# Kernel optimization log

Hardware: AMD Instinct MI355X
Metric: run time of the kernel (lower is better)

Reference implementation:

```python
import jax, jax.numpy as jnp
import numpy as np

NUM_ITERATIONS = 3


def _squash(s):
    # Faithful to the torch code: squash over dim=2 of s_j [B,1,nu,us,1],
    # which is the num_units axis. In our [B, nu, us] layout that is axis=1.
    mag_sq = jnp.sum(s ** 2, axis=1, keepdims=True)  # [B,1,us]
    mag = jnp.sqrt(mag_sq)
    return mag_sq / (1.0 + mag_sq) * (s / mag)


def setup_inputs() -> dict:
    key = jax.random.key(0)
    k1, k2 = jax.random.split(key)
    B, in_units, in_channels, num_units, unit_size = 256, 8, 1152, 10, 16
    x = jax.random.normal(k1, (B, in_units, in_channels), dtype=jnp.float32)
    W = jax.random.normal(k2, (1, in_channels, num_units, unit_size, in_units), dtype=jnp.float32)
    return {"x": x, "W": W}


def reference(x, W):
    B = x.shape[0]
    W0 = W[0]  # [ic, nu, us, iu]
    ic, nu = W0.shape[0], W0.shape[1]
    xt = jnp.swapaxes(x, 1, 2)  # [B, ic, iu]
    # u_hat = W @ x per (batch, in_channel, out_unit): [B, ic, nu, us]
    u_hat = jnp.einsum('cdui,bci->bcdu', W0, xt)
    b_ij = jnp.zeros((ic, nu), dtype=x.dtype)
    v = None
    for _ in range(NUM_ITERATIONS):
        c_ij = jax.nn.softmax(b_ij, axis=0)              # softmax over in_channels
        s_j = jnp.einsum('cd,bcdu->bdu', c_ij, u_hat)    # [B, nu, us]
        v = _squash(s_j)                                 # [B, nu, us]
        # agreement: <u_hat, v> over unit_size, mean over batch -> [ic, nu]
        agree = jnp.einsum('bcdu,bdu->cd', u_hat, v) / B
        b_ij = b_ij + agree
    return v  # [B, num_units, unit_size]
```

## Files before the change

### kernel.cpp

```cpp
#include <hip/hip_runtime.h>
#include <math.h>

#define B_  256
#define IU  8
#define IC  1152
#define NU  10
#define US  16
#define CCH 9
#define NCH 128
#define BT  64
#define NBLK 512
#define SPSTRIDE ((size_t)NCH * B_ * NU * US)

__device__ __forceinline__ float gld(const float* p) {
    return __hip_atomic_load(p, __ATOMIC_RELAXED, __HIP_MEMORY_SCOPE_AGENT);
}
__device__ __forceinline__ void gst(float* p, float v) {
    __hip_atomic_store(p, v, __ATOMIC_RELAXED, __HIP_MEMORY_SCOPE_AGENT);
}
__device__ __forceinline__ unsigned uld(const unsigned* p) {
    return __hip_atomic_load(p, __ATOMIC_RELAXED, __HIP_MEMORY_SCOPE_AGENT);
}
__device__ __forceinline__ void ust(unsigned* p, unsigned v) {
    __hip_atomic_store(p, v, __ATOMIC_RELAXED, __HIP_MEMORY_SCOPE_AGENT);
}

__device__ __forceinline__ void gridbar(unsigned* bar) {
    __syncthreads();
    if (threadIdx.x == 0) {
        const int bid = blockIdx.x;
        const int leaf = bid >> 3;
        const int mid  = bid >> 6;
        unsigned* myR1 = bar + (96 + leaf) * 32;
        unsigned g = uld(myR1);
        unsigned a = __hip_atomic_fetch_add(bar + leaf * 32, 1u,
                                            __ATOMIC_RELAXED, __HIP_MEMORY_SCOPE_AGENT);
        if (a == 7u) {
            ust(bar + leaf * 32, 0u);
            unsigned b2 = __hip_atomic_fetch_add(bar + (64 + mid) * 32, 1u,
                                                 __ATOMIC_RELAXED, __HIP_MEMORY_SCOPE_AGENT);
            if (b2 == 7u) {
                ust(bar + (64 + mid) * 32, 0u);
                unsigned c2 = __hip_atomic_fetch_add(bar + 72 * 32, 1u,
                                                     __ATOMIC_RELAXED, __HIP_MEMORY_SCOPE_AGENT);
                if (c2 == 7u) {
                    ust(bar + 72 * 32, 0u);
#pragma unroll
                    for (int k = 0; k < 8; k++)
                        ust(bar + (80 + k) * 32, g + 1u);
                }
                while (uld(bar + (80 + mid) * 32) == g)
                    __builtin_amdgcn_s_sleep(8);
#pragma unroll
                for (int j = 0; j < 8; j++)
                    ust(bar + (96 + mid * 8 + j) * 32, g + 1u);
            }
        }
        while (uld(myR1) == g)
            __builtin_amdgcn_s_sleep(16);
    }
    __syncthreads();
}

__global__ __launch_bounds__(256, 2) void mega(const float* __restrict__ x,
                                               const float* __restrict__ W,
                                               float* __restrict__ sp,
                                               float* __restrict__ vb0,
                                               float* __restrict__ vb1,
                                               float* __restrict__ bij,
                                               float* __restrict__ out,
                                               unsigned* __restrict__ bar) {
    __shared__ float4 ws[CCH * NU * 2 * 16];
    __shared__ __align__(16) float xs[CCH * BT * IU];
    __shared__ float aux[NU * US];
    __shared__ float cs[NU * CCH];

    const int tid = threadIdx.x;
    const int bid = blockIdx.x;
    const int grp = bid & 7;
    const int slot_ = bid >> 3;
    const int ch = ((slot_ >> 2) << 3) | grp;
    const int bt = slot_ & 3;
    const int b0 = bt * BT, c0 = ch * CCH;

    const float4* wg = (const float4*)W + (size_t)c0 * 320;
    for (int q = tid; q < CCH * NU * 32; q += 256) {
        int h = q & 1, u = (q >> 1) & 15, cd = q >> 5;
        ws[(cd * 2 + h) * 16 + u] = wg[q];
    }
    for (int idx = tid; idx < CCH * BT * IU; idx += 256) {
        int cc = idx % CCH;
        int r = idx / CCH;
        xs[cc * (BT * IU) + r] = x[((size_t)(b0 + (r >> 3)) * IU + (r & 7)) * IC + c0 + cc];
    }

    const int uq = tid & 15;
    const int bs = tid >> 4;
    const int wv = tid >> 6;
    const int lane = tid & 63;

    for (int iter = 0; iter < 3; ++iter) {
        float* spb = sp + (size_t)iter * SPSTRIDE;

        __syncthreads();
        if (iter == 0) {
            for (int q = tid; q < NU * CCH; q += 256) cs[q] = 1.0f;
        } else {
            for (int d = wv; d < NU; d += 4) {
                const float* brow = bij + (size_t)d * IC;
                float bv[18];
                float mx = -1e30f;
#pragma unroll
                for (int j = 0; j < 18; j++) {
                    bv[j] = gld(brow + lane + j * 64);
                    mx = fmaxf(mx, bv[j]);
                }
#pragma unroll
                for (int off = 32; off > 0; off >>= 1)
                    mx = fmaxf(mx, __shfl_xor(mx, off, 64));
                float sume = 0.0f;
#pragma unroll
                for (int j = 0; j < 18; j++) sume += expf(bv[j] - mx);
#pragma unroll
                for (int off = 32; off > 0; off >>= 1)
                    sume += __shfl_xor(sume, off, 64);
                const float inv = 1.0f / sume;
                if (lane < CCH)
                    cs[d * CCH + lane] = expf(gld(brow + c0 + lane) - mx) * inv;
            }
        }
        __syncthreads();
        const float scale = iter ? 1.0f : (1.0f / (float)IC);

        {
            float acc[4][NU];
#pragma unroll
            for (int bb = 0; bb < 4; bb++)
#pragma unroll
                for (int d = 0; d < NU; d++) acc[bb][d] = 0.0f;

#pragma unroll 3
            for (int cc = 0; cc < CCH; cc++) {
                float4 xv0[4], xv1[4];
#pragma unroll
                for (int bb = 0; bb < 4; bb++) {
                    const float4* xp = (const float4*)(xs + (cc * BT + bs + 16 * bb) * IU);
                    xv0[bb] = xp[0]; xv1[bb] = xp[1];
                }
#pragma unroll
                for (int d = 0; d < NU; d++) {
                    float4 w0 = ws[((cc * NU + d) * 2 + 0) * 16 + uq];
                    float4 w1 = ws[((cc * NU + d) * 2 + 1) * 16 + uq];
                    const float cw = cs[d * CCH + cc];
#pragma unroll
                    for (int bb = 0; bb < 4; bb++) {
                        float uh = w0.x * xv0[bb].x + w0.y * xv0[bb].y + w0.z * xv0[bb].z + w0.w * xv0[bb].w
                                 + w1.x * xv1[bb].x + w1.y * xv1[bb].y + w1.z * xv1[bb].z + w1.w * xv1[bb].w;
                        acc[bb][d] = fmaf(cw, uh, acc[bb][d]);
                    }
                }
            }
#pragma unroll
            for (int bb = 0; bb < 4; bb++) {
                const int b = b0 + bs + 16 * bb;
#pragma unroll
                for (int d = 0; d < NU; d++)
                    gst(spb + (((size_t)ch * B_ + b) * NU + d) * US + uq, acc[bb][d] * scale);
            }
        }
        gridbar(bar);

        if (bid < B_) {
            if (tid < 160) {
                const int part = tid & 3;
                const int sl = tid >> 2;
                const float4* s4p = (const float4*)spb;
                float4 a = make_float4(0.f, 0.f, 0.f, 0.f);
#pragma unroll 8
                for (int k = 0; k < 32; ++k) {
                    float4 t = s4p[((size_t)(part * 32 + k) * B_ + bid) * 40 + sl];
                    a.x += t.x; a.y += t.y; a.z += t.z; a.w += t.w;
                }
                a.x += __shfl_xor(a.x, 1, 64); a.y += __shfl_xor(a.y, 1, 64);
                a.z += __shfl_xor(a.z, 1, 64); a.w += __shfl_xor(a.w, 1, 64);
                a.x += __shfl_xor(a.x, 2, 64); a.y += __shfl_xor(a.y, 2, 64);
                a.z += __shfl_xor(a.z, 2, 64); a.w += __shfl_xor(a.w, 2, 64);
                if (part == 0) {
                    aux[sl * 4 + 0] = a.x; aux[sl * 4 + 1] = a.y;
                    aux[sl * 4 + 2] = a.z; aux[sl * 4 + 3] = a.w;
                }
            }
            __syncthreads();
            if (tid < NU * US) {
                float s = aux[tid];
                float msq = 0.0f;
#pragma unroll
                for (int dd = 0; dd < NU; dd++) {
                    float t = aux[dd * US + uq];
                    msq = fmaf(t, t, msq);
                }
                float f = msq / ((1.0f + msq) * sqrtf(msq));
                if (iter == 2)
                    out[(size_t)bid * (NU * US) + tid] = s * f;
                else {
                    float* vdst = (iter == 0) ? vb0 : vb1;
                    gst(vdst + (size_t)bid * (NU * US) + tid, s * f);
                }
            }
        }
        if (iter == 2) return;
        gridbar(bar);

        {
            const int cl = tid >> 4;
            const float* vb = (iter == 0) ? vb0 : vb1;
            if (cl < CCH) {
                float4 wA[NU], wB[NU];
#pragma unroll
                for (int d = 0; d < NU; d++) {
                    wA[d] = ws[((cl * NU + d) * 2 + 0) * 16 + uq];
                    wB[d] = ws[((cl * NU + d) * 2 + 1) * 16 + uq];
                }
                float accd[NU];
#pragma unroll
                for (int d = 0; d < NU; d++) accd[d] = 0.0f;
                const int bstag = (cl & 3) * 7;
#pragma unroll 4
                for (int blx = 0; blx < BT; blx++) {
                    const int bl = (blx + bstag) & 63;
                    const float* xp = xs + (cl * BT + bl) * IU;
                    float4 x0 = *(const float4*)xp;
                    float4 x1 = *(const float4*)(xp + 4);
                    const float* vp = vb + (size_t)(b0 + bl) * (NU * US) + uq;
#pragma unroll
                    for (int d = 0; d < NU; d++) {
                        float uh = wA[d].x * x0.x + wA[d].y * x0.y + wA[d].z * x0.z + wA[d].w * x0.w
                                 + wB[d].x * x1.x + wB[d].y * x1.y + wB[d].z * x1.z + wB[d].w * x1.w;
                        accd[d] = fmaf(uh, vp[d * US], accd[d]);
                    }
                }
#pragma unroll
                for (int d = 0; d < NU; d++) {
                    float a = accd[d];
                    a += __shfl_xor(a, 1, 64);
                    a += __shfl_xor(a, 2, 64);
                    a += __shfl_xor(a, 4, 64);
                    a += __shfl_xor(a, 8, 64);
                    if (uq == 0)
                        atomicAdd(bij + (size_t)d * IC + c0 + cl, a * (1.0f / (float)B_));
                }
            }
        }
        gridbar(bar);
    }
}

extern "C" void kernel_launch(void* const* d_in, const int* in_sizes, int n_in,
                              void* d_out, int out_size, void* d_ws, size_t ws_size,
                              hipStream_t stream) {
    (void)in_sizes; (void)n_in; (void)out_size; (void)ws_size;
    const float* x = (const float*)d_in[0];
    const float* W = (const float*)d_in[1];
    float* out = (float*)d_out;

    unsigned* bar = (unsigned*)d_ws;
    float* bij = (float*)d_ws + 5120;
    float* sp  = bij + (size_t)NU * IC;
    float* vb0 = sp + 3 * SPSTRIDE;
    float* vb1 = vb0 + (size_t)B_ * NU * US;

    hipMemsetAsync(d_ws, 0, 5120 * 4 + (size_t)NU * IC * 4, stream);
    mega<<<NBLK, 256, 0, stream>>>(x, W, sp, vb0, vb1, bij, out, bar);
}
```

Measured before the change: 193.1 us.

## Split squash reduction across all blocks and pad shared x rows

```diff
diff --git a/kernel.cpp b/kernel.cpp
--- a/kernel.cpp
+++ b/kernel.cpp
@@ -10,6 +10,7 @@
 #define NCH 128
 #define BT  64
 #define NBLK 512
+#define XSP 516
 #define SPSTRIDE ((size_t)NCH * B_ * NU * US)
 
 __device__ __forceinline__ float gld(const float* p) {
@@ -71,7 +72,7 @@
                                                float* __restrict__ out,
                                                unsigned* __restrict__ bar) {
     __shared__ float4 ws[CCH * NU * 2 * 16];
-    __shared__ __align__(16) float xs[CCH * BT * IU];
+    __shared__ __align__(16) float xs[CCH * XSP];
     __shared__ float aux[NU * US];
     __shared__ float cs[NU * CCH];
 
@@ -91,7 +92,7 @@
     for (int idx = tid; idx < CCH * BT * IU; idx += 256) {
         int cc = idx % CCH;
         int r = idx / CCH;
-        xs[cc * (BT * IU) + r] = x[((size_t)(b0 + (r >> 3)) * IU + (r & 7)) * IC + c0 + cc];
+        xs[cc * XSP + r] = x[((size_t)(b0 + (r >> 3)) * IU + (r & 7)) * IC + c0 + cc];
     }
 
     const int uq = tid & 15;
@@ -144,7 +145,7 @@
                 float4 xv0[4], xv1[4];
 #pragma unroll
                 for (int bb = 0; bb < 4; bb++) {
-                    const float4* xp = (const float4*)(xs + (cc * BT + bs + 16 * bb) * IU);
+                    const float4* xp = (const float4*)(xs + cc * XSP + (bs + 16 * bb) * IU);
                     xv0[bb] = xp[0]; xv1[bb] = xp[1];
                 }
 #pragma unroll
@@ -170,41 +171,52 @@
         }
         gridbar(bar);
 
-        if (bid < B_) {
+        {
+            const int batch = bid >> 1;
+            const int uh2 = bid & 1;
             if (tid < 160) {
-                const int part = tid & 3;
-                const int sl = tid >> 2;
+                const int part = tid & 7;
+                const int sl20 = tid >> 3;
+                const int dL = sl20 >> 1;
+                const int pr = sl20 & 1;
+                const int sl = dL * 4 + uh2 * 2 + pr;
                 const float4* s4p = (const float4*)spb;
                 float4 a = make_float4(0.f, 0.f, 0.f, 0.f);
-#pragma unroll 8
-                for (int k = 0; k < 32; ++k) {
-                    float4 t = s4p[((size_t)(part * 32 + k) * B_ + bid) * 40 + sl];
+#pragma unroll 4
+                for (int m = 0; m < 16; ++m) {
+                    float4 t = s4p[((size_t)(part + 8 * m) * B_ + batch) * 40 + sl];
                     a.x += t.x; a.y += t.y; a.z += t.z; a.w += t.w;
                 }
                 a.x += __shfl_xor(a.x, 1, 64); a.y += __shfl_xor(a.y, 1, 64);
                 a.z += __shfl_xor(a.z, 1, 64); a.w += __shfl_xor(a.w, 1, 64);
                 a.x += __shfl_xor(a.x, 2, 64); a.y += __shfl_xor(a.y, 2, 64);
                 a.z += __shfl_xor(a.z, 2, 64); a.w += __shfl_xor(a.w, 2, 64);
+                a.x += __shfl_xor(a.x, 4, 64); a.y += __shfl_xor(a.y, 4, 64);
+                a.z += __shfl_xor(a.z, 4, 64); a.w += __shfl_xor(a.w, 4, 64);
                 if (part == 0) {
-                    aux[sl * 4 + 0] = a.x; aux[sl * 4 + 1] = a.y;
-                    aux[sl * 4 + 2] = a.z; aux[sl * 4 + 3] = a.w;
+                    aux[dL * 8 + pr * 4 + 0] = a.x;
+                    aux[dL * 8 + pr * 4 + 1] = a.y;
+                    aux[dL * 8 + pr * 4 + 2] = a.z;
+                    aux[dL * 8 + pr * 4 + 3] = a.w;
                 }
             }
             __syncthreads();
-            if (tid < NU * US) {
-                float s = aux[tid];
+            if (tid < NU * 8) {
+                const int dL = tid >> 3, j = tid & 7;
+                float s = aux[dL * 8 + j];
                 float msq = 0.0f;
 #pragma unroll
                 for (int dd = 0; dd < NU; dd++) {
-                    float t = aux[dd * US + uq];
+                    float t = aux[dd * 8 + j];
                     msq = fmaf(t, t, msq);
                 }
                 float f = msq / ((1.0f + msq) * sqrtf(msq));
+                const size_t o = (size_t)batch * (NU * US) + dL * US + uh2 * 8 + j;
                 if (iter == 2)
-                    out[(size_t)bid * (NU * US) + tid] = s * f;
+                    out[o] = s * f;
                 else {
                     float* vdst = (iter == 0) ? vb0 : vb1;
-                    gst(vdst + (size_t)bid * (NU * US) + tid, s * f);
+                    gst(vdst + o, s * f);
                 }
             }
         }
@@ -228,7 +240,7 @@
 #pragma unroll 4
                 for (int blx = 0; blx < BT; blx++) {
                     const int bl = (blx + bstag) & 63;
-                    const float* xp = xs + (cl * BT + bl) * IU;
+                    const float* xp = xs + cl * XSP + bl * IU;
                     float4 x0 = *(const float4*)xp;
                     float4 x1 = *(const float4*)(xp + 4);
                     const float* vp = vb + (size_t)(b0 + bl) * (NU * US) + uq;
```

New measurement: 199.2 us. +3.2%, slower.
